# Optimization experiments

Measured on AMD Instinct MI355X. Metric: run time of the kernel, lower is better.

## Reference

```python
import jax, jax.numpy as jnp
import numpy as np

B, H, S, D = 2, 16, 2048, 128


def setup_inputs() -> dict:
    key = jax.random.key(0)
    kq, kk, kv = jax.random.split(key, 3)
    q1 = jax.random.normal(kq, (B, H, S, D), dtype=jnp.float32)
    k1 = jax.random.normal(kk, (B, H, S, D), dtype=jnp.float32)
    v1 = jax.random.normal(kv, (B, H, S, D), dtype=jnp.float32)
    scale_factor = jnp.float32(1.0 / np.sqrt(D))
    dropout_p = jnp.float32(0.5)
    return {"q1": q1, "k1": k1, "v1": v1, "scale_factor": scale_factor, "dropout_p": dropout_p}


def reference(q1, k1, v1, scale_factor, dropout_p):
    # scores: [B,H,S,S]
    qk = jnp.einsum("bhqd,bhkd->bhqk", q1, k1)
    softmax_qk = jax.nn.softmax(qk * scale_factor, axis=-1)
    # dropout (training mode, as in F.dropout default): keep w.p. 1-p, scale by 1/(1-p)
    keep = jax.random.bernoulli(jax.random.key(42), 1.0 - dropout_p, softmax_qk.shape)
    dropout_qk = jnp.where(keep, softmax_qk / (1.0 - dropout_p), 0.0)
    # output: [B,H,S,D]
    return jnp.einsum("bhqk,bhkd->bhqd", dropout_qk, v1)
```

## Files before the change

kernel.cpp:

```cpp
#include <hip/hip_runtime.h>

typedef float    f32x4  __attribute__((ext_vector_type(4)));
typedef __bf16   bf16x8 __attribute__((ext_vector_type(8)));
typedef unsigned int u32;
typedef unsigned int u32x4 __attribute__((ext_vector_type(4)));
typedef unsigned short u16;

#define S_LEN 2048
#define D_DIM 128
#define NHEAD 32
#define QBLK  128
#define KVBLK 64
#define NWAVE 8
#define WS_NEED (2u * NHEAD * S_LEN * D_DIM * 2u)

#define MEMFENCE() asm volatile("" ::: "memory")

__device__ __forceinline__ u32 rotl32(u32 x, int r) {
  return __builtin_amdgcn_alignbit(x, x, 32 - r);
}

__device__ __forceinline__ u32 threefry_bits(u32 ctr) {
  const u32 ks1 = 42u;
  const u32 ks2 = 0x1BD11BF0u;
  u32 x0 = 0u;
  u32 x1 = ctr + ks1;
#define TFR(r) { x0 += x1; x1 = rotl32(x1, (r)); x1 ^= x0; }
  TFR(13) TFR(15) TFR(26) TFR(6)
  x0 += ks1; x1 += ks2 + 1u;
  TFR(17) TFR(29) TFR(16) TFR(24)
  x0 += ks2; x1 += 2u;
  TFR(13) TFR(15) TFR(26) TFR(6)
  x1 += ks1 + 3u;
  TFR(17) TFR(29) TFR(16) TFR(24)
  x0 += ks1; x1 += ks2 + 4u;
  TFR(13) TFR(15) TFR(26) TFR(6)
  x0 += ks2; x1 += 5u;
#undef TFR
  return x0 ^ x1;
}

__device__ __forceinline__ u16 f2bf(float f) {
  u32 u = __float_as_uint(f);
  return (u16)((u + 0x7fffu + ((u >> 16) & 1u)) >> 16);
}

__device__ __forceinline__ u32 cvtpk(float lo, float hi) {
  u32 r;
  asm("v_cvt_pk_bf16_f32 %0, %1, %2" : "=v"(r) : "v"(lo), "v"(hi));
  return r;
}

__device__ __forceinline__ float exp2a(float x) {
  float r;
  asm("v_exp_f32 %0, %1" : "=v"(r) : "v"(x));
  return r;
}

__device__ __forceinline__ void gl_lds16(const void* g, void* l) {
  __builtin_amdgcn_global_load_lds(
      (const __attribute__((address_space(1))) void*)g,
      (__attribute__((address_space(3))) void*)l, 16, 0, 0);
}

__device__ __forceinline__ u32 swzv(int d) { return (u32)((d & 7) ^ ((d >> 2) & 7)); }

__global__ void __launch_bounds__(256) prepack(
    const float* __restrict__ Kp, const float* __restrict__ Vp,
    u16* __restrict__ kimg, u16* __restrict__ vimg)
{
  __shared__ u16 vt[KVBLK * D_DIM];
  const int blk = blockIdx.x;
  const int h = blk >> 5, tk = blk & 31;
  const float* Kh = Kp + ((size_t)h * S_LEN + (size_t)tk * KVBLK) * D_DIM;
  const float* Vh = Vp + ((size_t)h * S_LEN + (size_t)tk * KVBLK) * D_DIM;
  u16* kd = kimg + (size_t)blk * (KVBLK * D_DIM);
  u16* vd = vimg + (size_t)blk * (KVBLK * D_DIM);
  const int t = threadIdx.x;

#pragma unroll
  for (int it = 0; it < 4; ++it) {
    u32 p = (u32)(it * 256 + t) * 16;
    u32 krow = p >> 8;
    u32 cb = (p & 255) ^ ((krow & 7) << 4);
    const float* src = Kh + krow * D_DIM + (cb >> 1);
    f32x4 a = *(const f32x4*)(src);
    f32x4 b = *(const f32x4*)(src + 4);
    u32x4 o;
    o.x = cvtpk(a[0], a[1]); o.y = cvtpk(a[2], a[3]);
    o.z = cvtpk(b[0], b[1]); o.w = cvtpk(b[2], b[3]);
    *(u32x4*)((char*)kd + p) = o;
  }
#pragma unroll
  for (int it = 0; it < 8; ++it) {
    int g = it * 256 + t;
    int kv = g >> 5, d4 = g & 31;
    f32x4 x = *(const f32x4*)(Vh + (size_t)kv * D_DIM + d4 * 4);
    u32* dst = (u32*)(vt + kv * D_DIM + d4 * 4);
    dst[0] = cvtpk(x[0], x[1]);
    dst[1] = cvtpk(x[2], x[3]);
  }
  __syncthreads();
#pragma unroll
  for (int it = 0; it < 4; ++it) {
    u32 p = (u32)(it * 256 + t) * 16;
    u32 vdr = p >> 7;
    u32 cb = (p & 127) ^ (swzv((int)vdr) << 4);
    u32 kv0 = cb >> 1;
    u16 e[8];
#pragma unroll
    for (int i = 0; i < 8; ++i) e[i] = vt[(kv0 + i) * D_DIM + vdr];
    u32x4 o;
    o.x = (u32)e[0] | ((u32)e[1] << 16);
    o.y = (u32)e[2] | ((u32)e[3] << 16);
    o.z = (u32)e[4] | ((u32)e[5] << 16);
    o.w = (u32)e[6] | ((u32)e[7] << 16);
    *(u32x4*)((char*)vd + p) = o;
  }
}

__global__ void __launch_bounds__(512, 4) attn_fwd(
    const float* __restrict__ Qp, const u16* __restrict__ kimg,
    const u16* __restrict__ vimg, const float* __restrict__ scp,
    const float* __restrict__ dpp, float* __restrict__ Op)
{
  __shared__ alignas(16) u16 kbuf[KVBLK * D_DIM];
  __shared__ alignas(16) u16 vbuf[D_DIM * KVBLK];
  __shared__ alignas(16) u16 pbuf[NWAVE][16 * KVBLK];

  const int n    = blockIdx.x;
  const int head = ((n & 7) << 2) | ((n >> 3) & 3);
  const int qblk = n >> 5;
  const int t  = threadIdx.x;
  const int w  = t >> 6;
  const int l  = t & 63;
  const int lg = l >> 4;
  const int lc = l & 15;

  const float scale  = scp[0];
  const float keep_p = 1.0f - dpp[0];
  const float qmul   = scale * 1.44269504088896340736f;

  u32 ithr;
  {
    float T = keep_p * 8388608.0f;
    u32 Ti = (u32)T;
    u32 thr9 = ((float)Ti == T) ? Ti : (Ti + 1u);
    ithr = (thr9 >= (1u << 23)) ? 0xFFFFFFFFu : (thr9 << 9);
  }

  const float* __restrict__ Qh = Qp + (size_t)head * (S_LEN * D_DIM);
  float*       __restrict__ Oh = Op + (size_t)head * (S_LEN * D_DIM);
  const u16* __restrict__ kim = kimg + (size_t)head * 32 * (KVBLK * D_DIM);
  const u16* __restrict__ vim = vimg + (size_t)head * 32 * (KVBLK * D_DIM);

  bf16x8 qf[4];
  {
    const int qrow = qblk * QBLK + w * 16 + lc;
    const float* qsrc = Qh + (size_t)qrow * D_DIM + lg * 8;
#pragma unroll
    for (int kc = 0; kc < 4; ++kc) {
      f32x4 a = *(const f32x4*)(qsrc + kc * 32);
      f32x4 b = *(const f32x4*)(qsrc + kc * 32 + 4);
      union { u32 w4[4]; bf16x8 v; } uu;
      uu.w4[0] = cvtpk(a[0] * qmul, a[1] * qmul);
      uu.w4[1] = cvtpk(a[2] * qmul, a[3] * qmul);
      uu.w4[2] = cvtpk(b[0] * qmul, b[1] * qmul);
      uu.w4[3] = cvtpk(b[2] * qmul, b[3] * qmul);
      qf[kc] = uu.v;
    }
  }

  f32x4 acc[8];
#pragma unroll
  for (int dt = 0; dt < 8; ++dt) acc[dt] = f32x4{0.f, 0.f, 0.f, 0.f};
  float lrun[4] = { 0.f, 0.f, 0.f, 0.f };

  u16* pb = &pbuf[w][0];
  const u32 qrow_c0 = (u32)(qblk * QBLK + w * 16 + lg * 4);
  const u32 ibase0  = ((u32)head * S_LEN + qrow_c0) * S_LEN;

  for (int tkv = 0; tkv < S_LEN / KVBLK; ++tkv) {
    {
      const u16* kt_ = kim + (size_t)tkv * (KVBLK * D_DIM);
      const u16* vt_ = vim + (size_t)tkv * (KVBLK * D_DIM);
#pragma unroll
      for (int it = 0; it < 2; ++it) {
        int ck = it * 8 + w;
        gl_lds16((const char*)kt_ + ck * 1024 + l * 16, (char*)kbuf + ck * 1024);
        gl_lds16((const char*)vt_ + ck * 1024 + l * 16, (char*)vbuf + ck * 1024);
      }
    }
    __syncthreads();

    f32x4 sa[4];
#pragma unroll
    for (int ct = 0; ct < 4; ++ct) sa[ct] = f32x4{0.f, 0.f, 0.f, 0.f};
    __builtin_amdgcn_s_setprio(1);
#pragma unroll
    for (int kc = 0; kc < 4; ++kc) {
#pragma unroll
      for (int ct = 0; ct < 4; ++ct) {
        int krow = ct * 16 + lc;
        u32 koff = ((u32)(krow * 256 + (lg * 8 + kc * 32) * 2)) ^ ((u32)(krow & 7) << 4);
        bf16x8 kf = *(const bf16x8*)((char*)kbuf + koff);
        sa[ct] = __builtin_amdgcn_mfma_f32_16x16x32_bf16(qf[kc], kf, sa[ct], 0, 0, 0);
      }
    }
    __builtin_amdgcn_s_setprio(0);

#pragma unroll
    for (int j = 0; j < 4; ++j) {
      u32 ib = ibase0 + (u32)j * S_LEN + (u32)(tkv * KVBLK) + (u32)lc;
      float p0 = exp2a(sa[0][j]);
      float p1 = exp2a(sa[1][j]);
      float p2 = exp2a(sa[2][j]);
      float p3 = exp2a(sa[3][j]);
      lrun[j] += (p0 + p1) + (p2 + p3);
      u32 b0 = threefry_bits(ib);
      u32 b1 = threefry_bits(ib + 16u);
      u32 b2 = threefry_bits(ib + 32u);
      u32 b3 = threefry_bits(ib + 48u);
      float m0 = (b0 < ithr) ? p0 : 0.0f;
      float m1 = (b1 < ithr) ? p1 : 0.0f;
      float m2 = (b2 < ithr) ? p2 : 0.0f;
      float m3 = (b3 < ithr) ? p3 : 0.0f;
      u32 pk01 = cvtpk(m0, m1);
      u32 pk23 = cvtpk(m2, m3);
      int prow = lg * 4 + j;
      u32 rb = (u32)(prow * 128 + lc * 2);
      u32 sw = (u32)(prow & 7) << 4;
      *(u16*)((char*)pb + ((rb      ) ^ sw)) = (u16)pk01;
      *(u16*)((char*)pb + ((rb +  32) ^ sw)) = (u16)(pk01 >> 16);
      *(u16*)((char*)pb + ((rb +  64) ^ sw)) = (u16)pk23;
      *(u16*)((char*)pb + ((rb +  96) ^ sw)) = (u16)(pk23 >> 16);
    }

    MEMFENCE();
    __builtin_amdgcn_sched_barrier(0);

    __builtin_amdgcn_s_setprio(1);
#pragma unroll
    for (int kc2 = 0; kc2 < 2; ++kc2) {
      u32 poff = ((u32)(lc * 128 + (lg * 8 + kc2 * 32) * 2)) ^ ((u32)(lc & 7) << 4);
      bf16x8 pa = *(const bf16x8*)((char*)pb + poff);
#pragma unroll
      for (int dt = 0; dt < 8; ++dt) {
        int vd = dt * 16 + lc;
        u32 voff = ((u32)(vd * 128 + (lg * 8 + kc2 * 32) * 2)) ^ (swzv(vd) << 4);
        bf16x8 vb = *(const bf16x8*)((char*)vbuf + voff);
        acc[dt] = __builtin_amdgcn_mfma_f32_16x16x32_bf16(pa, vb, acc[dt], 0, 0, 0);
      }
    }
    __builtin_amdgcn_s_setprio(0);

    MEMFENCE();
    __syncthreads();
  }

#pragma unroll
  for (int j = 0; j < 4; ++j) {
    float ls = lrun[j];
    ls += __shfl_xor(ls, 1, 64);
    ls += __shfl_xor(ls, 2, 64);
    ls += __shfl_xor(ls, 4, 64);
    ls += __shfl_xor(ls, 8, 64);
    float sc = (1.0f / keep_p) / ls;
    u32 qg = qrow_c0 + (u32)j;
#pragma unroll
    for (int dt = 0; dt < 8; ++dt) {
      Oh[(size_t)qg * D_DIM + dt * 16 + lc] = acc[dt][j] * sc;
    }
  }
}

__global__ void __launch_bounds__(256) attn_fwd_fb(
    const float* __restrict__ Qp, const float* __restrict__ Kp,
    const float* __restrict__ Vp, const float* __restrict__ scp,
    const float* __restrict__ dpp, float* __restrict__ Op)
{
  __shared__ alignas(16) u16 kbuf[KVBLK * D_DIM];
  __shared__ alignas(16) u16 vbuf[D_DIM * KVBLK];
  __shared__ alignas(16) u16 pbuf[4][16 * KVBLK];

  const int n    = blockIdx.y * gridDim.x + blockIdx.x;
  const int head = ((n & 7) << 2) | ((n >> 3) & 3);
  const int qblk = n >> 5;
  const int t  = threadIdx.x;
  const int w  = t >> 6;
  const int l  = t & 63;
  const int lg = l >> 4;
  const int lc = l & 15;

  const float scale  = scp[0];
  const float keep_p = 1.0f - dpp[0];
  const float qmul   = scale * 1.44269504088896340736f;
  u32 ithr;
  {
    float T = keep_p * 8388608.0f;
    u32 Ti = (u32)T;
    u32 thr9 = ((float)Ti == T) ? Ti : (Ti + 1u);
    ithr = (thr9 >= (1u << 23)) ? 0xFFFFFFFFu : (thr9 << 9);
  }

  const float* __restrict__ Qh = Qp + (size_t)head * (S_LEN * D_DIM);
  const float* __restrict__ Kh = Kp + (size_t)head * (S_LEN * D_DIM);
  const float* __restrict__ Vh = Vp + (size_t)head * (S_LEN * D_DIM);
  float*       __restrict__ Oh = Op + (size_t)head * (S_LEN * D_DIM);

  bf16x8 qf[4];
  {
    const int qrow = qblk * 64 + w * 16 + lc;
    const float* qsrc = Qh + (size_t)qrow * D_DIM + lg * 8;
#pragma unroll
    for (int kc = 0; kc < 4; ++kc) {
      f32x4 a = *(const f32x4*)(qsrc + kc * 32);
      f32x4 b = *(const f32x4*)(qsrc + kc * 32 + 4);
      union { u16 h[8]; bf16x8 v; } uu;
#pragma unroll
      for (int i = 0; i < 4; ++i) {
        uu.h[i]     = f2bf(a[i] * qmul);
        uu.h[4 + i] = f2bf(b[i] * qmul);
      }
      qf[kc] = uu.v;
    }
  }

  f32x4 acc[8];
#pragma unroll
  for (int dt = 0; dt < 8; ++dt) acc[dt] = f32x4{0.f, 0.f, 0.f, 0.f};
  float lrun[4] = { 0.f, 0.f, 0.f, 0.f };

  u16* pb = &pbuf[w][0];
  const u32 qrow_c0 = (u32)(qblk * 64 + w * 16 + lg * 4);
  const u32 ibase0  = ((u32)head * S_LEN + qrow_c0) * S_LEN;

  for (int tkv = 0; tkv < S_LEN / KVBLK; ++tkv) {
#pragma unroll
    for (int r = 0; r < 8; ++r) {
      int g = r * 256 + t;
      int kv = g >> 5, d4 = g & 31;
      f32x4 x = *(const f32x4*)(Kh + (size_t)(tkv * KVBLK + kv) * D_DIM + d4 * 4);
      u32 w0 = (u32)f2bf(x[0]) | ((u32)f2bf(x[1]) << 16);
      u32 w1 = (u32)f2bf(x[2]) | ((u32)f2bf(x[3]) << 16);
      u32 off = ((u32)(kv * 256 + d4 * 8)) ^ ((u32)(kv & 7) << 4);
      u32* dst = (u32*)((char*)kbuf + off);
      dst[0] = w0; dst[1] = w1;
    }
#pragma unroll
    for (int r = 0; r < 8; ++r) {
      int rowloc = w * 16 + (r & 1) * 8 + (l >> 3);
      int d4     = (r >> 1) * 8 + (l & 7);
      f32x4 x = *(const f32x4*)(Vh + (size_t)(tkv * KVBLK + rowloc) * D_DIM + d4 * 4);
      u16 mb0 = f2bf(x[0]), mb1 = f2bf(x[1]), mb2 = f2bf(x[2]), mb3 = f2bf(x[3]);
      u16 pb0 = (u16)__shfl_xor((int)mb0, 8, 64);
      u16 pb1 = (u16)__shfl_xor((int)mb1, 8, 64);
      u16 pb2 = (u16)__shfl_xor((int)mb2, 8, 64);
      u16 pb3 = (u16)__shfl_xor((int)mb3, 8, 64);
      bool ev = ((l >> 3) & 1) == 0;
      int kvp = rowloc & ~1;
      u32 wA = ev ? ((u32)mb0 | ((u32)pb0 << 16)) : ((u32)pb2 | ((u32)mb2 << 16));
      u32 wB = ev ? ((u32)mb1 | ((u32)pb1 << 16)) : ((u32)pb3 | ((u32)mb3 << 16));
      int dA = d4 * 4 + (ev ? 0 : 2);
      u32 offA = ((u32)(dA * 128 + kvp * 2)) ^ (swzv(dA) << 4);
      u32 offB = ((u32)((dA + 1) * 128 + kvp * 2)) ^ (swzv(dA + 1) << 4);
      *(u32*)((char*)vbuf + offA) = wA;
      *(u32*)((char*)vbuf + offB) = wB;
    }
    __syncthreads();

    f32x4 sa[4];
#pragma unroll
    for (int ct = 0; ct < 4; ++ct) sa[ct] = f32x4{0.f, 0.f, 0.f, 0.f};
#pragma unroll
    for (int kc = 0; kc < 4; ++kc) {
#pragma unroll
      for (int ct = 0; ct < 4; ++ct) {
        int krow = ct * 16 + lc;
        u32 koff = ((u32)(krow * 256 + (lg * 8 + kc * 32) * 2)) ^ ((u32)(krow & 7) << 4);
        bf16x8 kf = *(const bf16x8*)((char*)kbuf + koff);
        sa[ct] = __builtin_amdgcn_mfma_f32_16x16x32_bf16(qf[kc], kf, sa[ct], 0, 0, 0);
      }
    }

#pragma unroll
    for (int j = 0; j < 4; ++j) {
      u32 ib = ibase0 + (u32)j * S_LEN + (u32)(tkv * KVBLK) + (u32)lc;
      float p0 = exp2a(sa[0][j]);
      float p1 = exp2a(sa[1][j]);
      float p2 = exp2a(sa[2][j]);
      float p3 = exp2a(sa[3][j]);
      lrun[j] += (p0 + p1) + (p2 + p3);
      u32 b0 = threefry_bits(ib);
      u32 b1 = threefry_bits(ib + 16u);
      u32 b2 = threefry_bits(ib + 32u);
      u32 b3 = threefry_bits(ib + 48u);
      float m0 = (b0 < ithr) ? p0 : 0.0f;
      float m1 = (b1 < ithr) ? p1 : 0.0f;
      float m2 = (b2 < ithr) ? p2 : 0.0f;
      float m3 = (b3 < ithr) ? p3 : 0.0f;
      u32 pk01 = cvtpk(m0, m1);
      u32 pk23 = cvtpk(m2, m3);
      int prow = lg * 4 + j;
      u32 rb = (u32)(prow * 128 + lc * 2);
      u32 sw = (u32)(prow & 7) << 4;
      *(u16*)((char*)pb + ((rb      ) ^ sw)) = (u16)pk01;
      *(u16*)((char*)pb + ((rb +  32) ^ sw)) = (u16)(pk01 >> 16);
      *(u16*)((char*)pb + ((rb +  64) ^ sw)) = (u16)pk23;
      *(u16*)((char*)pb + ((rb +  96) ^ sw)) = (u16)(pk23 >> 16);
    }
    asm volatile("" ::: "memory");

#pragma unroll
    for (int kc2 = 0; kc2 < 2; ++kc2) {
      u32 poff = ((u32)(lc * 128 + (lg * 8 + kc2 * 32) * 2)) ^ ((u32)(lc & 7) << 4);
      bf16x8 pa = *(const bf16x8*)((char*)pb + poff);
#pragma unroll
      for (int dt = 0; dt < 8; ++dt) {
        int vd = dt * 16 + lc;
        u32 voff = ((u32)(vd * 128 + (lg * 8 + kc2 * 32) * 2)) ^ (swzv(vd) << 4);
        bf16x8 vb = *(const bf16x8*)((char*)vbuf + voff);
        acc[dt] = __builtin_amdgcn_mfma_f32_16x16x32_bf16(pa, vb, acc[dt], 0, 0, 0);
      }
    }
    asm volatile("" ::: "memory");
    __syncthreads();
  }

#pragma unroll
  for (int j = 0; j < 4; ++j) {
    float ls = lrun[j];
    ls += __shfl_xor(ls, 1, 64);
    ls += __shfl_xor(ls, 2, 64);
    ls += __shfl_xor(ls, 4, 64);
    ls += __shfl_xor(ls, 8, 64);
    float sc = (1.0f / keep_p) / ls;
    u32 qg = qrow_c0 + (u32)j;
#pragma unroll
    for (int dt = 0; dt < 8; ++dt) {
      Oh[(size_t)qg * D_DIM + dt * 16 + lc] = acc[dt][j] * sc;
    }
  }
}

extern "C" void kernel_launch(void* const* d_in, const int* in_sizes, int n_in,
                              void* d_out, int out_size, void* d_ws, size_t ws_size,
                              hipStream_t stream) {
  const float* q  = (const float*)d_in[0];
  const float* k  = (const float*)d_in[1];
  const float* v  = (const float*)d_in[2];
  const float* sc = (const float*)d_in[3];
  const float* dp = (const float*)d_in[4];
  float* out = (float*)d_out;
  if (ws_size >= (size_t)WS_NEED) {
    u16* kimg = (u16*)d_ws;
    u16* vimg = kimg + (size_t)NHEAD * S_LEN * D_DIM;
    hipLaunchKernelGGL(prepack, dim3(NHEAD * (S_LEN / KVBLK)), dim3(256), 0, stream, k, v, kimg, vimg);
    hipLaunchKernelGGL(attn_fwd, dim3(NHEAD * (S_LEN / QBLK)), dim3(512), 0, stream,
                       q, kimg, vimg, sc, dp, out);
  } else {
    hipLaunchKernelGGL(attn_fwd_fb, dim3(S_LEN / 64, NHEAD), dim3(256), 0, stream, q, k, v, sc, dp, out);
  }
}
```

Measured before the change: 323.0 us.

## Double-buffer K/V LDS tiles to prefetch next tile during compute

Doubles the K and V shared-memory buffers and issues the direct-to-LDS loads for the next KV tile before computing on the current one. This removes the per-iteration barrier that made every iteration wait for its own tile's global loads, so load latency can overlap with the QK MFMAs, dropout RNG and PV MFMAs. It raises shared memory per block from about 48KB to 80KB. With 512 blocks spread over the CUs that probably does not reduce resident blocks, but it could limit occupancy in other configurations.

New measurement: 335.4 us. +3.8%, slower.

```diff
diff --git a/kernel.cpp b/kernel.cpp
--- a/kernel.cpp
+++ b/kernel.cpp
@@ -124,8 +124,8 @@
     const u16* __restrict__ vimg, const float* __restrict__ scp,
     const float* __restrict__ dpp, float* __restrict__ Op)
 {
-  __shared__ alignas(16) u16 kbuf[KVBLK * D_DIM];
-  __shared__ alignas(16) u16 vbuf[D_DIM * KVBLK];
+  __shared__ alignas(16) u16 kbuf[2][KVBLK * D_DIM];
+  __shared__ alignas(16) u16 vbuf[2][D_DIM * KVBLK];
   __shared__ alignas(16) u16 pbuf[NWAVE][16 * KVBLK];
 
   const int n    = blockIdx.x;
@@ -180,18 +180,24 @@
   const u32 qrow_c0 = (u32)(qblk * QBLK + w * 16 + lg * 4);
   const u32 ibase0  = ((u32)head * S_LEN + qrow_c0) * S_LEN;
 
+#define STAGE_TILE(BUF, TKV)                                                      \
+  {                                                                               \
+    const u16* kt_ = kim + (size_t)(TKV) * (KVBLK * D_DIM);                       \
+    const u16* vt_ = vim + (size_t)(TKV) * (KVBLK * D_DIM);                       \
+    _Pragma("unroll")                                                             \
+    for (int it = 0; it < 2; ++it) {                                              \
+      int ck = it * 8 + w;                                                        \
+      gl_lds16((const char*)kt_ + ck * 1024 + l * 16, (char*)kbuf[BUF] + ck * 1024); \
+      gl_lds16((const char*)vt_ + ck * 1024 + l * 16, (char*)vbuf[BUF] + ck * 1024); \
+    }                                                                             \
+  }
+
+  STAGE_TILE(0, 0)
+  __syncthreads();
+
   for (int tkv = 0; tkv < S_LEN / KVBLK; ++tkv) {
-    {
-      const u16* kt_ = kim + (size_t)tkv * (KVBLK * D_DIM);
-      const u16* vt_ = vim + (size_t)tkv * (KVBLK * D_DIM);
-#pragma unroll
-      for (int it = 0; it < 2; ++it) {
-        int ck = it * 8 + w;
-        gl_lds16((const char*)kt_ + ck * 1024 + l * 16, (char*)kbuf + ck * 1024);
-        gl_lds16((const char*)vt_ + ck * 1024 + l * 16, (char*)vbuf + ck * 1024);
-      }
-    }
-    __syncthreads();
+    const int cur = tkv & 1;
+    if (tkv + 1 < S_LEN / KVBLK) STAGE_TILE(cur ^ 1, tkv + 1)
 
     f32x4 sa[4];
 #pragma unroll
@@ -203,7 +209,7 @@
       for (int ct = 0; ct < 4; ++ct) {
         int krow = ct * 16 + lc;
         u32 koff = ((u32)(krow * 256 + (lg * 8 + kc * 32) * 2)) ^ ((u32)(krow & 7) << 4);
-        bf16x8 kf = *(const bf16x8*)((char*)kbuf + koff);
+        bf16x8 kf = *(const bf16x8*)((char*)kbuf[cur] + koff);
         sa[ct] = __builtin_amdgcn_mfma_f32_16x16x32_bf16(qf[kc], kf, sa[ct], 0, 0, 0);
       }
     }
@@ -248,7 +254,7 @@
       for (int dt = 0; dt < 8; ++dt) {
         int vd = dt * 16 + lc;
         u32 voff = ((u32)(vd * 128 + (lg * 8 + kc2 * 32) * 2)) ^ (swzv(vd) << 4);
-        bf16x8 vb = *(const bf16x8*)((char*)vbuf + voff);
+        bf16x8 vb = *(const bf16x8*)((char*)vbuf[cur] + voff);
         acc[dt] = __builtin_amdgcn_mfma_f32_16x16x32_bf16(pa, vb, acc[dt], 0, 0, 0);
       }
     }
@@ -257,6 +263,7 @@
     MEMFENCE();
     __syncthreads();
   }
+#undef STAGE_TILE
 
 #pragma unroll
   for (int j = 0; j < 4; ++j) {
```
